# Optimization experiments

Measured on AMD Instinct MI355X. Metric: run time of the kernel, lower is better.

The kernel has to match this reference:

```python
import jax, jax.numpy as jnp
import numpy as np

HH, WW = 7, 7  # pooled output size (module init: height, width)


def setup_inputs() -> dict:
    key = jax.random.key(0)
    k1, k2, k3, k4, k5 = jax.random.split(key, 5)
    C, Hf, Wf = 512, 64, 256        # conv feature map (stride 8)
    B = 4096                        # number of RoI boxes
    img_h, img_w = 512, 2048        # original image size
    feats = jax.random.normal(k1, (C, Hf, Wf), dtype=jnp.float32)
    w = jax.random.uniform(k2, (B,), minval=16.0, maxval=256.0)
    h = jax.random.uniform(k3, (B,), minval=16.0, maxval=128.0)
    xc = jax.random.uniform(k4, (B,), minval=0.0, maxval=float(img_w))
    yc = jax.random.uniform(k5, (B,), minval=0.0, maxval=float(img_h))
    boxes = jnp.stack([xc, yc, w, h], axis=1).astype(jnp.float32)  # (B,4) xc,yc,w,h in image coords
    return {"feats": feats, "boxes": boxes, "img_height": img_h, "img_width": img_w}


def _bilinear_sample(feats, px, py):
    """feats: (C,Hf,Wf); px,py: (B,HH,WW) pixel coords in feature map. Zero padding outside."""
    C, Hf, Wf = feats.shape
    x0 = jnp.floor(px)
    y0 = jnp.floor(py)
    x1 = x0 + 1.0
    y1 = y0 + 1.0
    wx1 = px - x0
    wx0 = 1.0 - wx1
    wy1 = py - y0
    wy0 = 1.0 - wy1

    def gather(xi, yi):
        valid = (xi >= 0) & (xi <= Wf - 1) & (yi >= 0) & (yi <= Hf - 1)
        xi_c = jnp.clip(xi, 0, Wf - 1).astype(jnp.int32)
        yi_c = jnp.clip(yi, 0, Hf - 1).astype(jnp.int32)
        v = feats[:, yi_c, xi_c]                     # (C,B,HH,WW)
        return v * valid[None].astype(feats.dtype)

    out = (gather(x0, y0) * (wx0 * wy0)[None]
           + gather(x1, y0) * (wx1 * wy0)[None]
           + gather(x0, y1) * (wx0 * wy1)[None]
           + gather(x1, y1) * (wx1 * wy1)[None])    # (C,B,HH,WW)
    return jnp.transpose(out, (1, 0, 2, 3))          # (B,C,HH,WW)


def reference(feats, boxes, img_height, img_width):
    # box_to_affine (densecap BoxToAffine, align_corners=True normalization) fused
    # with affine_grid: sample coords computed inline per box.
    B = boxes.shape[0]
    C, Hf, Wf = feats.shape
    xc, yc, w, h = boxes[:, 0], boxes[:, 1], boxes[:, 2], boxes[:, 3]
    tx = jnp.linspace(-1.0, 1.0, WW, dtype=feats.dtype)
    ty = jnp.linspace(-1.0, 1.0, HH, dtype=feats.dtype)
    inv_w = 1.0 / (img_width - 1)
    inv_h = 1.0 / (img_height - 1)
    # normalized image coords: gx = (2*xc-(W-1))/(W-1) + tx * w/(W-1)
    gx = (2.0 * xc[:, None] - (img_width - 1)) * inv_w + (w * inv_w)[:, None] * tx[None, :]   # (B,WW)
    gy = (2.0 * yc[:, None] - (img_height - 1)) * inv_h + (h * inv_h)[:, None] * ty[None, :]  # (B,HH)
    # map normalized [-1,1] to feature-map pixel coords (align_corners=True)
    px = (gx + 1.0) * 0.5 * (Wf - 1)
    py = (gy + 1.0) * 0.5 * (Hf - 1)
    px = jnp.broadcast_to(px[:, None, :], (B, HH, WW))
    py = jnp.broadcast_to(py[:, :, None], (B, HH, WW))
    return _bilinear_sample(feats, px, py)            # (B,C,HH,WW)
```

## Files before the change

### kernel.cpp

```cpp
#include <hip/hip_runtime.h>
#include <math.h>

#define HH 7
#define WW 7
#define CC 512
#define HF 64
#define WF 256
#define NS 49
#define CHUNK 128
#define ROWS4 (CC / 4)
#define NE4 ((CHUNK * NS) / 4)

typedef float floatv4 __attribute__((ext_vector_type(4)));

__global__ __launch_bounds__(256) void transpose_feats(const float* __restrict__ in,
                                                       float* __restrict__ out) {
    __shared__ float tile[32][33];
    const int P = HF * WF;
    int p  = blockIdx.x * 32 + threadIdx.x;
    int cb = blockIdx.y * 32;
#pragma unroll
    for (int r = 0; r < 32; r += 8)
        tile[threadIdx.y + r][threadIdx.x] = in[(size_t)(cb + threadIdx.y + r) * P + p];
    __syncthreads();
    int c  = cb + threadIdx.x;
    int pb = blockIdx.x * 32;
#pragma unroll
    for (int r = 0; r < 32; r += 8)
        out[(size_t)(pb + threadIdx.y + r) * CC + c] = tile[threadIdx.x][threadIdx.y + r];
}

__device__ __forceinline__ void box_setup(int s, int b,
                                          const float* __restrict__ boxes,
                                          const int* __restrict__ ih_p,
                                          const int* __restrict__ iw_p,
                                          int4* o_out, float4* w_out) {
    int i = s / WW;
    int j = s - i * WW;
    float IW1 = (float)(iw_p[0] - 1);
    float IH1 = (float)(ih_p[0] - 1);
    float xc = boxes[b * 4 + 0];
    float yc = boxes[b * 4 + 1];
    float bw = boxes[b * 4 + 2];
    float bh = boxes[b * 4 + 3];
    float inv_w = 1.0f / IW1;
    float inv_h = 1.0f / IH1;
    float tx = (float)(j - 3) * (1.0f / 3.0f);
    float ty = (float)(i - 3) * (1.0f / 3.0f);
    float gx = (2.0f * xc - IW1) * inv_w + (bw * inv_w) * tx;
    float gy = (2.0f * yc - IH1) * inv_h + (bh * inv_h) * ty;
    float px = (gx + 1.0f) * 0.5f * (float)(WF - 1);
    float py = (gy + 1.0f) * 0.5f * (float)(HF - 1);

    float x0f = floorf(px), y0f = floorf(py);
    float wx1 = px - x0f, wx0 = 1.0f - wx1;
    float wy1 = py - y0f, wy0 = 1.0f - wy1;
    float x1f = x0f + 1.0f, y1f = y0f + 1.0f;

    bool vx0 = (x0f >= 0.0f) && (x0f <= (float)(WF - 1));
    bool vx1 = (x1f >= 0.0f) && (x1f <= (float)(WF - 1));
    bool vy0 = (y0f >= 0.0f) && (y0f <= (float)(HF - 1));
    bool vy1 = (y1f >= 0.0f) && (y1f <= (float)(HF - 1));

    int xi0 = (int)fminf(fmaxf(x0f, 0.0f), (float)(WF - 1));
    int xi1 = (int)fminf(fmaxf(x1f, 0.0f), (float)(WF - 1));
    int yi0 = (int)fminf(fmaxf(y0f, 0.0f), (float)(HF - 1));
    int yi1 = (int)fminf(fmaxf(y1f, 0.0f), (float)(HF - 1));

    int4 o;
    o.x = yi0 * WF + xi0;
    o.y = yi0 * WF + xi1;
    o.z = yi1 * WF + xi0;
    o.w = yi1 * WF + xi1;
    float4 w4;
    w4.x = wx0 * wy0 * ((vx0 && vy0) ? 1.0f : 0.0f);
    w4.y = wx1 * wy0 * ((vx1 && vy0) ? 1.0f : 0.0f);
    w4.z = wx0 * wy1 * ((vx0 && vy1) ? 1.0f : 0.0f);
    w4.w = wx1 * wy1 * ((vx1 && vy1) ? 1.0f : 0.0f);
    *o_out = o;
    *w_out = w4;
}

__global__ __launch_bounds__(256) void roi_pool_v3(const float* __restrict__ src,
                                                   const float* __restrict__ boxes,
                                                   const int* __restrict__ ih_p,
                                                   const int* __restrict__ iw_p,
                                                   float* __restrict__ out) {
    __shared__ int4   s_off[NS];
    __shared__ float4 s_wt[NS];
    __shared__ float  tile[CHUNK * 64];

    const int b   = blockIdx.x;
    const int tid = threadIdx.x;
    const int g   = tid & 31;
    const int h   = tid >> 5;

    if (tid < NS) {
        int4 o; float4 w4;
        box_setup(tid, b, boxes, ih_p, iw_p, &o, &w4);
        o.x *= ROWS4; o.y *= ROWS4; o.z *= ROWS4; o.w *= ROWS4;
        s_off[tid] = o;
        s_wt[tid]  = w4;
    }
    __syncthreads();

    int4   o_r[7];
    float4 w_r[7];
    int    sig_r[7];
#pragma unroll
    for (int it = 0; it < 7; ++it) {
        int s = h + (it << 3);
        if (s < NS) {
            o_r[it]   = s_off[s];
            w_r[it]   = s_wt[s];
            sig_r[it] = (s >> 2) | ((s & 3) << 4);
        }
    }

    const size_t outbase = (size_t)b * (CC * NS);
    const float4* src4   = (const float4*)src;

    for (int c0 = 0; c0 < CC; c0 += CHUNK) {
        const int cb4 = c0 >> 2;
#pragma unroll
        for (int it = 0; it < 7; ++it) {
            int s = h + (it << 3);
            if (s < NS) {
                int4   o = o_r[it];
                float4 w = w_r[it];
                float4 a  = src4[o.x + cb4 + g];
                float4 bb = src4[o.y + cb4 + g];
                float4 c  = src4[o.z + cb4 + g];
                float4 d  = src4[o.w + cb4 + g];
                int base = g << 8;
                int sw   = sig_r[it] ^ g;
                tile[base +       sw] = a.x * w.x + bb.x * w.y + c.x * w.z + d.x * w.w;
                tile[base +  64 + sw] = a.y * w.x + bb.y * w.y + c.y * w.z + d.y * w.w;
                tile[base + 128 + sw] = a.z * w.x + bb.z * w.y + c.z * w.z + d.z * w.w;
                tile[base + 192 + sw] = a.w * w.x + bb.w * w.y + c.w * w.z + d.w * w.w;
            }
        }
        __syncthreads();
        float* outc = out + outbase + (size_t)c0 * NS;
        for (int k4 = tid; k4 < NE4; k4 += 256) {
            int e = k4 << 2;
            int c = e / NS;
            int s = e - c * NS;
            floatv4 v;
            v.x = tile[(c << 6) + (((s >> 2) | ((s & 3) << 4)) ^ (c >> 2))];
            if (++s == NS) { s = 0; ++c; }
            v.y = tile[(c << 6) + (((s >> 2) | ((s & 3) << 4)) ^ (c >> 2))];
            if (++s == NS) { s = 0; ++c; }
            v.z = tile[(c << 6) + (((s >> 2) | ((s & 3) << 4)) ^ (c >> 2))];
            if (++s == NS) { s = 0; ++c; }
            v.w = tile[(c << 6) + (((s >> 2) | ((s & 3) << 4)) ^ (c >> 2))];
            __builtin_nontemporal_store(v, (floatv4*)outc + k4);
        }
        __syncthreads();
    }
}

__global__ __launch_bounds__(256) void roi_pool_fb(const float* __restrict__ src,
                                                   const float* __restrict__ boxes,
                                                   const int* __restrict__ ih_p,
                                                   const int* __restrict__ iw_p,
                                                   float* __restrict__ out) {
    __shared__ int4   s_off[NS];
    __shared__ float4 s_wt[NS];
    __shared__ float  tile[NS * 257];

    const int b   = blockIdx.x;
    const int tid = threadIdx.x;

    if (tid < NS) {
        int4 o; float4 w4;
        box_setup(tid, b, boxes, ih_p, iw_p, &o, &w4);
        s_off[tid] = o;
        s_wt[tid]  = w4;
    }
    __syncthreads();

    const size_t outbase = (size_t)b * (CC * NS);
    for (int c0 = 0; c0 < CC; c0 += 256) {
        const int cterm = (c0 + tid) * (HF * WF);
        for (int s = 0; s < NS; ++s) {
            int4   o = s_off[s];
            float4 w = s_wt[s];
            float v = src[o.x + cterm] * w.x + src[o.y + cterm] * w.y +
                      src[o.z + cterm] * w.z + src[o.w + cterm] * w.w;
            tile[s * 257 + tid] = v;
        }
        __syncthreads();
        const size_t ob = outbase + (size_t)c0 * NS;
        for (int k = tid; k < 256 * NS; k += 256) {
            int cl = k / NS;
            int s  = k - cl * NS;
            out[ob + k] = tile[s * 257 + cl];
        }
        __syncthreads();
    }
}

extern "C" void kernel_launch(void* const* d_in, const int* in_sizes, int n_in,
                              void* d_out, int out_size, void* d_ws, size_t ws_size,
                              hipStream_t stream) {
    const float* feats = (const float*)d_in[0];
    const float* boxes = (const float*)d_in[1];
    const int*   ih    = (const int*)d_in[2];
    const int*   iw    = (const int*)d_in[3];
    float*       out   = (float*)d_out;
    const int B = in_sizes[1] / 4;

    const size_t need = (size_t)CC * HF * WF * sizeof(float);
    if (ws_size >= need) {
        float* tf = (float*)d_ws;
        dim3 tb(32, 8);
        dim3 tg((HF * WF) / 32, CC / 32);
        transpose_feats<<<tg, tb, 0, stream>>>(feats, tf);
        roi_pool_v3<<<B, 256, 0, stream>>>(tf, boxes, ih, iw, out);
    } else {
        roi_pool_fb<<<B, 256, 0, stream>>>(feats, boxes, ih, iw, out);
    }
}
```

Before: 537.4 us.

## Sort boxes spatially and assign contiguous sorted ranges to each XCD

Adds a single-block counting-sort kernel that bins boxes by center on a serpentine 32x64 grid and writes a permutation. The pooling kernel maps each block id to a rank so that each of the 8 XCDs processes a contiguous run of spatially nearby boxes. This is meant to improve L2 reuse of the transposed feature map within each XCD. The cost is an extra serial launch and a dependent index load per block. The output is unchanged because each block still writes to its own box's slot.

```diff
diff --git a/kernel.cpp b/kernel.cpp
--- a/kernel.cpp
+++ b/kernel.cpp
@@ -10,6 +10,7 @@
 #define CHUNK 128
 #define ROWS4 (CC / 4)
 #define NE4 ((CHUNK * NS) / 4)
+#define NBINS 2048
 
 typedef float floatv4 __attribute__((ext_vector_type(4)));
 
@@ -28,6 +29,54 @@
 #pragma unroll
     for (int r = 0; r < 32; r += 8)
         out[(size_t)(pb + threadIdx.y + r) * CC + c] = tile[threadIdx.x][threadIdx.y + r];
+}
+
+__device__ __forceinline__ int box_key(const float* __restrict__ boxes, int b,
+                                       float sy, float sx) {
+    float xc = boxes[b * 4 + 0];
+    float yc = boxes[b * 4 + 1];
+    int yb = (int)(yc * sy);
+    int xb = (int)(xc * sx);
+    yb = min(max(yb, 0), 31);
+    xb = min(max(xb, 0), 63);
+    if (yb & 1) xb = 63 - xb;
+    return (yb << 6) | xb;
+}
+
+__global__ __launch_bounds__(256) void sort_boxes(const float* __restrict__ boxes,
+                                                  const int* __restrict__ ih_p,
+                                                  const int* __restrict__ iw_p,
+                                                  int B, int* __restrict__ perm) {
+    __shared__ int hist[NBINS];
+    __shared__ int part[256];
+    const int tid = threadIdx.x;
+    const float sy = 32.0f / (float)ih_p[0];
+    const float sx = 64.0f / (float)iw_p[0];
+
+    for (int i = tid; i < NBINS; i += 256) hist[i] = 0;
+    __syncthreads();
+    for (int b = tid; b < B; b += 256)
+        atomicAdd(&hist[box_key(boxes, b, sy, sx)], 1);
+    __syncthreads();
+    const int base = tid * (NBINS / 256);
+    int s = 0;
+#pragma unroll
+    for (int i = 0; i < NBINS / 256; ++i) { int v = hist[base + i]; hist[base + i] = s; s += v; }
+    part[tid] = s;
+    __syncthreads();
+    if (tid == 0) {
+        int acc = 0;
+        for (int t = 0; t < 256; ++t) { int v = part[t]; part[t] = acc; acc += v; }
+    }
+    __syncthreads();
+    const int off = part[tid];
+#pragma unroll
+    for (int i = 0; i < NBINS / 256; ++i) hist[base + i] += off;
+    __syncthreads();
+    for (int b = tid; b < B; b += 256) {
+        int pos = atomicAdd(&hist[box_key(boxes, b, sy, sx)], 1);
+        perm[pos] = b;
+    }
 }
 
 __device__ __forceinline__ void box_setup(int s, int b,
@@ -81,16 +130,23 @@
     *w_out = w4;
 }
 
-__global__ __launch_bounds__(256) void roi_pool_v3(const float* __restrict__ src,
+__global__ __launch_bounds__(256) void roi_pool_v4(const float* __restrict__ src,
                                                    const float* __restrict__ boxes,
                                                    const int* __restrict__ ih_p,
                                                    const int* __restrict__ iw_p,
+                                                   const int* __restrict__ perm,
                                                    float* __restrict__ out) {
     __shared__ int4   s_off[NS];
     __shared__ float4 s_wt[NS];
     __shared__ float  tile[CHUNK * 64];
 
-    const int b   = blockIdx.x;
+    const int nwg  = gridDim.x;
+    const int bid  = blockIdx.x;
+    const int q    = nwg >> 3, r = nwg & 7;
+    const int xcd  = bid & 7, slot = bid >> 3;
+    const int rank = xcd * q + min(xcd, r) + slot;
+    const int b    = perm[rank];
+
     const int tid = threadIdx.x;
     const int g   = tid & 31;
     const int h   = tid >> 5;
@@ -211,13 +267,16 @@
     float*       out   = (float*)d_out;
     const int B = in_sizes[1] / 4;
 
-    const size_t need = (size_t)CC * HF * WF * sizeof(float);
+    const size_t tf_bytes = (size_t)CC * HF * WF * sizeof(float);
+    const size_t need = tf_bytes + (size_t)B * sizeof(int);
     if (ws_size >= need) {
-        float* tf = (float*)d_ws;
+        float* tf   = (float*)d_ws;
+        int*   perm = (int*)((char*)d_ws + tf_bytes);
         dim3 tb(32, 8);
         dim3 tg((HF * WF) / 32, CC / 32);
         transpose_feats<<<tg, tb, 0, stream>>>(feats, tf);
-        roi_pool_v3<<<B, 256, 0, stream>>>(tf, boxes, ih, iw, out);
+        sort_boxes<<<1, 256, 0, stream>>>(boxes, ih, iw, B, perm);
+        roi_pool_v4<<<B, 256, 0, stream>>>(tf, boxes, ih, iw, perm, out);
     } else {
         roi_pool_fb<<<B, 256, 0, stream>>>(feats, boxes, ih, iw, out);
     }
```

Measured after the change: 473.5 us. 1.13x faster.
